# Kernel optimization log

Measured on AMD Instinct MI355X. Metric: run time of the kernel, lower is better.

The kernel has to match this reference:

```python
import jax, jax.numpy as jnp
import numpy as np
from jax import lax

B, D, K = 256, 128, 8192


def _conv_same(x, w, b):
    # x: [B,C,H,W], w: [O,I,3,3] (torch Conv2d layout), stride 1, padding 1 == SAME
    y = lax.conv_general_dilated(x, w, (1, 1), 'SAME',
                                 dimension_numbers=('NCHW', 'OIHW', 'NCHW'))
    return y + b[None, :, None, None]


def _convT_same(x, w, b):
    # torch ConvTranspose2d(k=3, stride=1, padding=1) with weight [I,O,3,3]
    # == SAME conv with spatially flipped kernel and swapped in/out channels
    wt = jnp.flip(w, axis=(2, 3)).transpose(1, 0, 2, 3)  # -> [O,I,3,3]
    return _conv_same(x, wt, b)


def setup_inputs() -> dict:
    key = jax.random.key(0)
    ks = jax.random.split(key, 12)
    s = 0.05
    return {
        'patch':  jax.random.normal(ks[0], (B, 3, 64, 64), jnp.float32),
        'enc_w1': jax.random.normal(ks[1], (64, 3, 3, 3), jnp.float32) * s,
        'enc_b1': jnp.zeros((64,), jnp.float32),
        'enc_w2': jax.random.normal(ks[2], (D, 64, 3, 3), jnp.float32) * s,
        'enc_b2': jnp.zeros((D,), jnp.float32),
        'emb':    jax.random.normal(ks[3], (K, D), jnp.float32),
        'dec_w1': jax.random.normal(ks[4], (D, 64, 3, 3), jnp.float32) * s,  # ConvT [in,out,k,k]
        'dec_b1': jnp.zeros((64,), jnp.float32),
        'dec_w2': jax.random.normal(ks[5], (64, 64, 3, 3), jnp.float32) * s,
        'dec_b2': jnp.zeros((64,), jnp.float32),
        'dec_w3': jax.random.normal(ks[6], (64, 3, 3, 3), jnp.float32) * s,
        'dec_b3': jnp.zeros((3,), jnp.float32),
    }


def reference(patch, enc_w1, enc_b1, enc_w2, enc_b2, emb,
              dec_w1, dec_b1, dec_w2, dec_b2, dec_w3, dec_b3):
    # ---- encode_patch ----
    h = jax.nn.relu(_conv_same(patch, enc_w1, enc_b1))
    h = _conv_same(h, enc_w2, enc_b2)
    z = jnp.mean(h, axis=(2, 3))  # AdaptiveAvgPool2d((1,1)) + flatten -> [B,D]

    # ---- VQ: cdist + argmin + gather ----
    # argmin over squared L2 == argmin over cdist(p=2); avoid sqrt.
    d2 = (jnp.sum(z * z, axis=1, keepdims=True)
          + jnp.sum(emb * emb, axis=1)[None, :]
          - 2.0 * z @ emb.T)  # [B,K]
    encoding_indices = jnp.argmin(d2, axis=1)  # [B]
    z_q = emb[encoding_indices]  # [B,D]

    commitment_loss = jnp.mean((lax.stop_gradient(z_q) - z) ** 2)
    codebook_loss = jnp.mean((z_q - lax.stop_gradient(z)) ** 2)

    # ---- decode_vector ----
    # bilinear interpolate of a 1x1 map to 64x64 is a pure broadcast
    v = jnp.broadcast_to(z_q[:, :, None, None], (z_q.shape[0], z_q.shape[1], 64, 64))
    d = jax.nn.relu(_convT_same(v, dec_w1, dec_b1))
    d = jax.nn.relu(_convT_same(d, dec_w2, dec_b2))
    recon = jnp.tanh(_convT_same(d, dec_w3, dec_b3))  # [B,3,64,64]

    return recon, codebook_loss, commitment_loss, encoding_indices[:, None]
```

## Files before the change

### kernel.cpp

```cpp
#include <hip/hip_runtime.h>
#include <math.h>

typedef float float4u __attribute__((ext_vector_type(4), aligned(4)));


__global__ __launch_bounds__(512) void k_conv_z(
    const float* __restrict__ patch, const float* __restrict__ w1,
    const float* __restrict__ b1, const float* __restrict__ w2,
    const float* __restrict__ b2, const float* __restrict__ dw1,
    const float* __restrict__ emb,
    float* __restrict__ z, float* __restrict__ zn2,
    float* __restrict__ Wcfg, float* __restrict__ en2)
{
    __shared__ __align__(16) float lds[14256];
    const int blk = blockIdx.x, tid = threadIdx.x;

    if (blk >= 256) {
        const int gid = (blk - 256) * 512 + tid;
        if (gid < 73728) {
            const int cfg = gid >> 13;
            const int o = (gid >> 7) & 63;
            const int i = gid & 127;
            const int cy = cfg / 3, cx = cfg % 3;
            const int ylo = (cy == 2) ? 1 : 0, yhi = (cy == 0) ? 1 : 2;
            const int xlo = (cx == 2) ? 1 : 0, xhi = (cx == 0) ? 1 : 2;
            const float* wp = dw1 + ((size_t)i * 64 + o) * 9;
            float s = 0.f;
            for (int ky = ylo; ky <= yhi; ++ky)
                for (int kx = xlo; kx <= xhi; ++kx)
                    s += wp[ky * 3 + kx];
            Wcfg[gid] = s;
        } else {
            const int k = gid - 73728;
            const float4* e = (const float4*)(emb + (size_t)k * 128);
            float s = 0.f;
            for (int t = 0; t < 32; ++t) {
                const float4 v = e[t];
                s = fmaf(v.x, v.x, fmaf(v.y, v.y, fmaf(v.z, v.z, fmaf(v.w, v.w, s))));
            }
            en2[k] = s;
        }
        return;
    }

    const float* pb = patch + (size_t)blk * 12288;
    for (int i = tid; i < 14256; i += 512) {
        const int c = i / 4752, rem = i - c * 4752;
        const int r = rem / 72, p = rem - r * 72;
        const int y = r - 1, x = p - 3;
        float v = 0.f;
        if (y >= 0 && y < 64 && x >= 0 && x < 64)
            v = pb[(c << 12) + (y << 6) + x];
        lds[i] = v;
    }
    __syncthreads();

    const int ch = tid & 63, q = tid >> 6;
    float w[3][3][3];
#pragma unroll
    for (int ic = 0; ic < 3; ++ic)
#pragma unroll
        for (int ky = 0; ky < 3; ++ky)
#pragma unroll
            for (int kx = 0; kx < 3; ++kx)
                w[ic][ky][kx] = w1[((ch * 3 + ic) * 3 + ky) * 3 + kx];
    const float bias = b1[ch];

    float T = 0, r0s = 0, r63s = 0, c0s = 0, c63s = 0;
    float h00 = 0, h063 = 0, h630 = 0, h6363 = 0;

#pragma unroll 1
    for (int r8 = 0; r8 < 8; ++r8) {
        const int y = q * 8 + r8;
#pragma unroll 1
        for (int m = 0; m < 8; ++m) {
            float a[8];
#pragma unroll
            for (int j = 0; j < 8; ++j) a[j] = bias;
#pragma unroll
            for (int ic = 0; ic < 3; ++ic)
#pragma unroll
                for (int ky = 0; ky < 3; ++ky) {
                    const float* rowp = &lds[(ic * 66 + y + ky) * 72 + m * 8 + 2];
                    const float2 f01 = *(const float2*)rowp;
                    const float4 f25 = *(const float4*)(rowp + 2);
                    const float4 f69 = *(const float4*)(rowp + 6);
                    const float f[10] = {f01.x, f01.y, f25.x, f25.y, f25.z, f25.w,
                                         f69.x, f69.y, f69.z, f69.w};
                    const float w0 = w[ic][ky][0], w1v = w[ic][ky][1], w2v = w[ic][ky][2];
#pragma unroll
                    for (int j = 0; j < 8; ++j)
                        a[j] = fmaf(w0, f[j], fmaf(w1v, f[j + 1], fmaf(w2v, f[j + 2], a[j])));
                }
#pragma unroll
            for (int j = 0; j < 8; ++j) a[j] = fmaxf(a[j], 0.f);
            const float rs = ((a[0] + a[1]) + (a[2] + a[3])) + ((a[4] + a[5]) + (a[6] + a[7]));
            T += rs;
            if (y == 0)  { r0s += rs;  if (m == 0) h00 = a[0];  if (m == 7) h063 = a[7]; }
            if (y == 63) { r63s += rs; if (m == 0) h630 = a[0]; if (m == 7) h6363 = a[7]; }
            if (m == 0) c0s += a[0];
            if (m == 7) c63s += a[7];
        }
    }
    __syncthreads();

    {
        const float st[9] = {T, r0s, r63s, c0s, c63s, h00, h063, h630, h6363};
#pragma unroll
        for (int s = 0; s < 9; ++s) lds[(s * 8 + q) * 64 + ch] = st[s];
    }
    __syncthreads();

    float* Ssh = lds + 4608;
    if (tid < 64) {
        float f[9];
#pragma unroll
        for (int s = 0; s < 9; ++s) {
            float v = 0.f;
#pragma unroll
            for (int g = 0; g < 8; ++g) v += lds[(s * 8 + g) * 64 + tid];
            f[s] = v;
        }
        const float Tt = f[0], R0 = f[1], R63 = f[2], C0 = f[3], C63 = f[4];
        const float H00 = f[5], H063 = f[6], H630 = f[7], H6363 = f[8];
#pragma unroll
        for (int ky = 0; ky < 3; ++ky) {
            const float rex = (ky == 0) ? R63 : (ky == 2 ? R0 : 0.f);
#pragma unroll
            for (int kx = 0; kx < 3; ++kx) {
                const float cex = (kx == 0) ? C63 : (kx == 2 ? C0 : 0.f);
                float corner = 0.f;
                if (ky == 0 && kx == 0) corner = H6363;
                if (ky == 0 && kx == 2) corner = H630;
                if (ky == 2 && kx == 0) corner = H063;
                if (ky == 2 && kx == 2) corner = H00;
                Ssh[tid * 9 + ky * 3 + kx] = (Tt - rex - cex + corner) * (1.f / 4096.f);
            }
        }
    }
    __syncthreads();

    float* zp = lds + 5184;
    {
        const int oc = tid & 127, h = tid >> 7;
        const float4* Wv = (const float4*)(w2 + (size_t)oc * 576 + h * 144);
        const float4* Sv = (const float4*)(Ssh + h * 144);
        float acc = 0.f;
        for (int t = 0; t < 36; ++t) {
            const float4 w4 = Wv[t], s4 = Sv[t];
            acc = fmaf(w4.x, s4.x, acc);
            acc = fmaf(w4.y, s4.y, acc);
            acc = fmaf(w4.z, s4.z, acc);
            acc = fmaf(w4.w, s4.w, acc);
        }
        zp[tid] = acc;
    }
    __syncthreads();
    float* red2 = lds + 5696;
    if (tid < 128) {
        const float zv = b2[tid] + ((zp[tid] + zp[tid + 128]) + (zp[tid + 256] + zp[tid + 384]));
        z[(size_t)blk * 128 + tid] = zv;
        red2[tid] = zv * zv;
    }
    __syncthreads();
    if (tid < 64) {
        float v = red2[tid] + red2[tid + 64];
        v += __shfl_xor(v, 32); v += __shfl_xor(v, 16); v += __shfl_xor(v, 8);
        v += __shfl_xor(v, 4);  v += __shfl_xor(v, 2);  v += __shfl_xor(v, 1);
        if (tid == 0) zn2[blk] = v;
    }
}

__global__ __launch_bounds__(256) void k_vq(
    const float* __restrict__ z, const float* __restrict__ emb,
    const float* __restrict__ en2, float* __restrict__ pd2, int* __restrict__ pidx)
{
    __shared__ __align__(16) float zsh[1024];
    __shared__ float wd[8][4];
    __shared__ int   wi[8][4];
    const int tid = threadIdx.x;
    const int bg = blockIdx.x >> 4, kc = blockIdx.x & 15;
    const int b0 = bg * 8;
    for (int i = tid; i < 1024; i += 256) zsh[i] = z[(size_t)b0 * 128 + i];
    __syncthreads();

    const int k0 = kc * 512 + tid, k1 = k0 + 256;
    const float4* e0 = (const float4*)(emb + (size_t)k0 * 128);
    const float4* e1 = (const float4*)(emb + (size_t)k1 * 128);
    const float4* zv = (const float4*)zsh;

    float acc0[8], acc1[8];
#pragma unroll
    for (int bb = 0; bb < 8; ++bb) { acc0[bb] = 0.f; acc1[bb] = 0.f; }

    for (int t = 0; t < 32; ++t) {
        const float4 ea = e0[t], eb = e1[t];
#pragma unroll
        for (int bb = 0; bb < 8; ++bb) {
            const float4 zz = zv[bb * 32 + t];
            acc0[bb] = fmaf(zz.x, ea.x, fmaf(zz.y, ea.y, fmaf(zz.z, ea.z, fmaf(zz.w, ea.w, acc0[bb]))));
            acc1[bb] = fmaf(zz.x, eb.x, fmaf(zz.y, eb.y, fmaf(zz.z, eb.z, fmaf(zz.w, eb.w, acc1[bb]))));
        }
    }
    const float E0 = en2[k0], E1 = en2[k1];
    const int wv_ = tid >> 6, ln = tid & 63;
#pragma unroll
    for (int bb = 0; bb < 8; ++bb) {
        const float da = fmaf(-2.f, acc0[bb], E0);
        const float db = fmaf(-2.f, acc1[bb], E1);
        float d; int ix;
        if (da <= db) { d = da; ix = k0; } else { d = db; ix = k1; }
#pragma unroll
        for (int off = 32; off > 0; off >>= 1) {
            const float od = __shfl_xor(d, off);
            const int   oi = __shfl_xor(ix, off);
            if (od < d || (od == d && oi < ix)) { d = od; ix = oi; }
        }
        if (ln == 0) { wd[bb][wv_] = d; wi[bb][wv_] = ix; }
    }
    __syncthreads();
    if (tid < 8) {
        float d = wd[tid][0]; int ix = wi[tid][0];
#pragma unroll
        for (int wv2 = 1; wv2 < 4; ++wv2) {
            const float od = wd[tid][wv2]; const int oi = wi[tid][wv2];
            if (od < d || (od == d && oi < ix)) { d = od; ix = oi; }
        }
        pd2[(b0 + tid) * 16 + kc] = d;
        pidx[(b0 + tid) * 16 + kc] = ix;
    }
}

__global__ __launch_bounds__(256) void k_stage1(
    const float* __restrict__ emb, const float* __restrict__ zn2,
    const float* __restrict__ pd2, const int* __restrict__ pidx,
    const float* __restrict__ Wcfg, const float* __restrict__ db1,
    float* __restrict__ d1all, float* __restrict__ out)
{
    __shared__ float wsl[64 * 132];
    __shared__ float zql[8 * 132];
    __shared__ int   bish[8];
    __shared__ float redl[256];
    const int tid = threadIdx.x;
    const int g = blockIdx.x / 9, c = blockIdx.x - g * 9;
    const int b0 = g * 8;

    float dmin = pd2[tid * 16]; int bi = pidx[tid * 16];
    for (int j = 1; j < 16; ++j) {
        const float d = pd2[tid * 16 + j]; const int ix = pidx[tid * 16 + j];
        if (d < dmin || (d == dmin && ix < bi)) { dmin = d; bi = ix; }
    }
    if (tid >= b0 && tid < b0 + 8) bish[tid - b0] = bi;
    redl[tid] = dmin + zn2[tid];
    __syncthreads();
    if (blockIdx.x == 0) out[3145730 + tid] = (float)bi;
    if (tid < 128) redl[tid] += redl[tid + 128];
    __syncthreads();
    if (tid < 64) {
        float v = redl[tid] + redl[tid + 64];
        v += __shfl_xor(v, 32); v += __shfl_xor(v, 16); v += __shfl_xor(v, 8);
        v += __shfl_xor(v, 4);  v += __shfl_xor(v, 2);  v += __shfl_xor(v, 1);
        if (tid == 0 && blockIdx.x == 0) {
            const float L = v * (1.f / 32768.f);
            out[3145728] = L;
            out[3145729] = L;
        }
    }

    for (int idx = tid; idx < 2048; idx += 256) {
        const int o = idx >> 5, k4 = idx & 31;
        *(float4*)&wsl[o * 132 + k4 * 4] =
            *(const float4*)&Wcfg[((size_t)c * 64 + o) * 128 + k4 * 4];
    }
    {
        const int b = tid >> 5, k4 = tid & 31;
        *(float4*)&zql[b * 132 + k4 * 4] =
            *(const float4*)&emb[(size_t)bish[b] * 128 + k4 * 4];
    }
    __syncthreads();

#pragma unroll
    for (int pp = 0; pp < 2; ++pp) {
        const int pair = tid + pp * 256;
        const int o = pair >> 3, bb = pair & 7;
        const float4* wv = (const float4*)&wsl[o * 132];
        const float4* zv = (const float4*)&zql[bb * 132];
        float acc = db1[o];
        for (int t = 0; t < 32; ++t) {
            const float4 w4 = wv[t], z4 = zv[t];
            acc = fmaf(w4.x, z4.x, acc);
            acc = fmaf(w4.y, z4.y, acc);
            acc = fmaf(w4.z, z4.z, acc);
            acc = fmaf(w4.w, z4.w, acc);
        }
        d1all[((size_t)(b0 + bb)) * 576 + o * 9 + c] = fmaxf(acc, 0.f);
    }
}

__global__ __launch_bounds__(256) void k_decode(
    const float* __restrict__ d1all, const float* __restrict__ dw2,
    const float* __restrict__ db2, const float* __restrict__ dw3,
    const float* __restrict__ db3, float* __restrict__ out)
{
    __shared__ float d1e[64][10];
    __shared__ float d2e[64][26];
    __shared__ float o3[3 * 49];
    __shared__ float dw3sh[1728];

    const int b = blockIdx.x, tid = threadIdx.x;
    for (int id = tid; id < 576; id += 256) d1e[id / 9][id % 9] = d1all[(size_t)b * 576 + id];
    for (int id = tid; id < 1728; id += 256) dw3sh[id] = dw3[id];
    if (tid < 64) { d1e[tid][9] = 0.f; d2e[tid][25] = 0.f; }
    __syncthreads();

    {
        const int TY5[5][3] = {{-1,0,1},{0,1,1},{1,1,1},{1,1,2},{1,2,-1}};
        const int o = tid >> 2, isub = tid & 3;
        float acc[25];
#pragma unroll
        for (int cc = 0; cc < 25; ++cc) acc[cc] = 0.f;
        for (int ii = 0; ii < 16; ++ii) {
            const int i = isub + ii * 4;
            float d1v[10];
#pragma unroll
            for (int t = 0; t < 9; ++t) d1v[t] = d1e[i][t];
            d1v[9] = 0.f;
            const float* wp = dw2 + ((size_t)i * 64 + o) * 9;
            const float4u w03 = *(const float4u*)wp;
            const float4u w47 = *(const float4u*)(wp + 4);
            const float w8v = wp[8];
            const float w9[9] = {w03.x, w03.y, w03.z, w03.w, w47.x, w47.y, w47.z, w47.w, w8v};
#pragma unroll
            for (int cy = 0; cy < 5; ++cy) {
#pragma unroll
                for (int ky = 0; ky < 3; ++ky) {
                    const int ty = TY5[cy][ky];
                    if (ty < 0) continue;
#pragma unroll
                    for (int cx = 0; cx < 5; ++cx) {
#pragma unroll
                        for (int kx = 0; kx < 3; ++kx) {
                            const int tx = TY5[cx][kx];
                            if (tx < 0) continue;
                            acc[cy * 5 + cx] = fmaf(w9[(2 - ky) * 3 + (2 - kx)],
                                                    d1v[ty * 3 + tx], acc[cy * 5 + cx]);
                        }
                    }
                }
            }
        }
#pragma unroll
        for (int cc = 0; cc < 25; ++cc) {
            float v = acc[cc];
            v += __shfl_xor(v, 1);
            v += __shfl_xor(v, 2);
            if (isub == 0) d2e[o][cc] = fmaxf(v + db2[o], 0.f);
        }
    }
    __syncthreads();

    if (tid < 147) {
        const int TY7[7][3] = {{-1,0,1},{0,1,2},{1,2,2},{2,2,2},{2,2,3},{2,3,4},{3,4,-1}};
        const int c3 = tid / 49, cc = tid % 49, cy = cc / 7, cx = cc % 7;
        float acc = db3[c3];
        for (int i = 0; i < 64; ++i) {
            const float* wp = &dw3sh[(i * 3 + c3) * 9];
#pragma unroll
            for (int ky = 0; ky < 3; ++ky) {
                const int ty = TY7[cy][ky];
#pragma unroll
                for (int kx = 0; kx < 3; ++kx) {
                    const int tx = TY7[cx][kx];
                    const int t = (ty < 0 || tx < 0) ? 25 : ty * 5 + tx;
                    acc = fmaf(wp[(2 - ky) * 3 + (2 - kx)], d2e[i][t], acc);
                }
            }
        }
        o3[c3 * 49 + cc] = tanhf(acc);
    }
    __syncthreads();

    float4* ob = (float4*)(out + (size_t)b * 12288);
    for (int id = tid; id < 3072; id += 256) {
        const int base = id * 4;
        const int c = base >> 12, rem = base & 4095, y = rem >> 6, x0 = rem & 63;
        const int ry = (y <= 3) ? y : (y >= 60 ? y - 57 : 3);
        const float* row = &o3[c * 49 + ry * 7];
        float4 v;
        int x;
        x = x0 + 0; v.x = row[(x <= 3) ? x : (x >= 60 ? x - 57 : 3)];
        x = x0 + 1; v.y = row[(x <= 3) ? x : (x >= 60 ? x - 57 : 3)];
        x = x0 + 2; v.z = row[(x <= 3) ? x : (x >= 60 ? x - 57 : 3)];
        x = x0 + 3; v.w = row[(x <= 3) ? x : (x >= 60 ? x - 57 : 3)];
        ob[id] = v;
    }
}

extern "C" void kernel_launch(void* const* d_in, const int* in_sizes, int n_in,
                              void* d_out, int out_size, void* d_ws, size_t ws_size,
                              hipStream_t stream)
{
    const float* patch  = (const float*)d_in[0];
    const float* enc_w1 = (const float*)d_in[1];
    const float* enc_b1 = (const float*)d_in[2];
    const float* enc_w2 = (const float*)d_in[3];
    const float* enc_b2 = (const float*)d_in[4];
    const float* emb    = (const float*)d_in[5];
    const float* dec_w1 = (const float*)d_in[6];
    const float* dec_b1 = (const float*)d_in[7];
    const float* dec_w2 = (const float*)d_in[8];
    const float* dec_b2 = (const float*)d_in[9];
    const float* dec_w3 = (const float*)d_in[10];
    const float* dec_b3 = (const float*)d_in[11];

    float* out = (float*)d_out;
    float* ws  = (float*)d_ws;

    float* z     = ws;
    float* zn2   = ws + 32768;
    float* pd2   = ws + 33024;
    int*   pidx  = (int*)(ws + 37120);
    float* Wcfg  = ws + 41216;
    float* en2   = ws + 114944;
    float* d1all = ws + 123136;

    k_conv_z<<<dim3(416), dim3(512), 0, stream>>>(patch, enc_w1, enc_b1, enc_w2, enc_b2,
                                                  dec_w1, emb, z, zn2, Wcfg, en2);
    k_vq<<<dim3(512), dim3(256), 0, stream>>>(z, emb, en2, pd2, pidx);
    k_stage1<<<dim3(288), dim3(256), 0, stream>>>(emb, zn2, pd2, pidx, Wcfg, dec_b1,
                                                  d1all, out);
    k_decode<<<dim3(256), dim3(256), 0, stream>>>(d1all, dec_w2, dec_b2, dec_w3,
                                                  dec_b3, out);
}
```

Measured before the change: 146.8 us.

## Split encoder conv across four row-group blocks and fuse stage1 into decode

The first encoder conv is now split so each image is handled by four 256-thread blocks, one per 16-row group. Each block writes partial statistics to a workspace buffer, and the last block to finish (found via an atomic counter) reduces them and computes z. The conv inner loop is re-tiled to compute 4x4 output register tiles with row reuse. The separate stage1 kernel is merged into the decode kernel, which drops one launch and the d1all round trip, at the cost of per-sample redundant argmin reduction and a matvec that reads Wcfg straight from global memory. A memset is added to reset the counters.

```diff
diff --git a/kernel.cpp b/kernel.cpp
--- a/kernel.cpp
+++ b/kernel.cpp
@@ -4,19 +4,21 @@
 typedef float float4u __attribute__((ext_vector_type(4), aligned(4)));
 
 
-__global__ __launch_bounds__(512) void k_conv_z(
+__global__ __launch_bounds__(256, 3) void k_conv_z(
     const float* __restrict__ patch, const float* __restrict__ w1,
     const float* __restrict__ b1, const float* __restrict__ w2,
     const float* __restrict__ b2, const float* __restrict__ dw1,
     const float* __restrict__ emb,
+    float* __restrict__ pstat, int* __restrict__ cnt,
     float* __restrict__ z, float* __restrict__ zn2,
     float* __restrict__ Wcfg, float* __restrict__ en2)
 {
-    __shared__ __align__(16) float lds[14256];
+    __shared__ __align__(16) float lds[3888];
+    __shared__ int winflag;
     const int blk = blockIdx.x, tid = threadIdx.x;
 
-    if (blk >= 256) {
-        const int gid = (blk - 256) * 512 + tid;
+    if (blk >= 1024) {
+        const int gid = (blk - 1024) * 256 + tid;
         if (gid < 73728) {
             const int cfg = gid >> 13;
             const int o = (gid >> 7) & 63;
@@ -30,7 +32,7 @@
                 for (int kx = xlo; kx <= xhi; ++kx)
                     s += wp[ky * 3 + kx];
             Wcfg[gid] = s;
-        } else {
+        } else if (gid < 81920) {
             const int k = gid - 73728;
             const float4* e = (const float4*)(emb + (size_t)k * 128);
             float s = 0.f;
@@ -43,11 +45,13 @@
         return;
     }
 
-    const float* pb = patch + (size_t)blk * 12288;
-    for (int i = tid; i < 14256; i += 512) {
-        const int c = i / 4752, rem = i - c * 4752;
+    const int b = blk >> 2, rg = blk & 3;
+    const int y0 = rg * 16;
+    const float* pb = patch + (size_t)b * 12288;
+    for (int i = tid; i < 3888; i += 256) {
+        const int c = i / 1296, rem = i - c * 1296;
         const int r = rem / 72, p = rem - r * 72;
-        const int y = r - 1, x = p - 3;
+        const int y = y0 + r - 1, x = p - 3;
         float v = 0.f;
         if (y >= 0 && y < 64 && x >= 0 && x < 64)
             v = pb[(c << 12) + (y << 6) + x];
@@ -56,73 +60,99 @@
     __syncthreads();
 
     const int ch = tid & 63, q = tid >> 6;
-    float w[3][3][3];
+    float wgt[3][3][3];
 #pragma unroll
     for (int ic = 0; ic < 3; ++ic)
 #pragma unroll
         for (int ky = 0; ky < 3; ++ky)
 #pragma unroll
             for (int kx = 0; kx < 3; ++kx)
-                w[ic][ky][kx] = w1[((ch * 3 + ic) * 3 + ky) * 3 + kx];
+                wgt[ic][ky][kx] = w1[((ch * 3 + ic) * 3 + ky) * 3 + kx];
     const float bias = b1[ch];
+    const bool top = (rg == 0) && (q == 0);
+    const bool bot = (rg == 3) && (q == 3);
 
     float T = 0, r0s = 0, r63s = 0, c0s = 0, c63s = 0;
     float h00 = 0, h063 = 0, h630 = 0, h6363 = 0;
+    const float* tb = lds + q * 288;
 
 #pragma unroll 1
-    for (int r8 = 0; r8 < 8; ++r8) {
-        const int y = q * 8 + r8;
-#pragma unroll 1
-        for (int m = 0; m < 8; ++m) {
-            float a[8];
-#pragma unroll
-            for (int j = 0; j < 8; ++j) a[j] = bias;
-#pragma unroll
-            for (int ic = 0; ic < 3; ++ic)
-#pragma unroll
-                for (int ky = 0; ky < 3; ++ky) {
-                    const float* rowp = &lds[(ic * 66 + y + ky) * 72 + m * 8 + 2];
-                    const float2 f01 = *(const float2*)rowp;
-                    const float4 f25 = *(const float4*)(rowp + 2);
-                    const float4 f69 = *(const float4*)(rowp + 6);
-                    const float f[10] = {f01.x, f01.y, f25.x, f25.y, f25.z, f25.w,
-                                         f69.x, f69.y, f69.z, f69.w};
-                    const float w0 = w[ic][ky][0], w1v = w[ic][ky][1], w2v = w[ic][ky][2];
-#pragma unroll
-                    for (int j = 0; j < 8; ++j)
-                        a[j] = fmaf(w0, f[j], fmaf(w1v, f[j + 1], fmaf(w2v, f[j + 2], a[j])));
+    for (int xc = 0; xc < 16; ++xc) {
+        const float* bp = tb + xc * 4;
+        float acc[4][4];
+#pragma unroll
+        for (int dr = 0; dr < 4; ++dr)
+#pragma unroll
+            for (int j = 0; j < 4; ++j) acc[dr][j] = bias;
+
+#pragma unroll
+        for (int ic = 0; ic < 3; ++ic) {
+#pragma unroll
+            for (int rr = 0; rr < 6; ++rr) {
+                const float2 f01 = *(const float2*)(bp + (ic * 18 + rr) * 72 + 2);
+                const float4 f25 = *(const float4*)(bp + (ic * 18 + rr) * 72 + 4);
+                const float w6[6] = {f01.x, f01.y, f25.x, f25.y, f25.z, f25.w};
+#pragma unroll
+                for (int dr = 0; dr < 4; ++dr) {
+                    const int ky = rr - dr;
+                    if (ky >= 0 && ky < 3) {
+                        const float wa = wgt[ic][ky][0], wb = wgt[ic][ky][1], wc = wgt[ic][ky][2];
+#pragma unroll
+                        for (int j = 0; j < 4; ++j)
+                            acc[dr][j] = fmaf(wa, w6[j], fmaf(wb, w6[j + 1],
+                                          fmaf(wc, w6[j + 2], acc[dr][j])));
+                    }
                 }
-#pragma unroll
-            for (int j = 0; j < 8; ++j) a[j] = fmaxf(a[j], 0.f);
-            const float rs = ((a[0] + a[1]) + (a[2] + a[3])) + ((a[4] + a[5]) + (a[6] + a[7]));
-            T += rs;
-            if (y == 0)  { r0s += rs;  if (m == 0) h00 = a[0];  if (m == 7) h063 = a[7]; }
-            if (y == 63) { r63s += rs; if (m == 0) h630 = a[0]; if (m == 7) h6363 = a[7]; }
-            if (m == 0) c0s += a[0];
-            if (m == 7) c63s += a[7];
-        }
+            }
+        }
+        float rs[4];
+#pragma unroll
+        for (int dr = 0; dr < 4; ++dr) {
+#pragma unroll
+            for (int j = 0; j < 4; ++j) acc[dr][j] = fmaxf(acc[dr][j], 0.f);
+            rs[dr] = (acc[dr][0] + acc[dr][1]) + (acc[dr][2] + acc[dr][3]);
+            T += rs[dr];
+        }
+        if (xc == 0)  c0s  += (acc[0][0] + acc[1][0]) + (acc[2][0] + acc[3][0]);
+        if (xc == 15) c63s += (acc[0][3] + acc[1][3]) + (acc[2][3] + acc[3][3]);
+        if (top) { r0s += rs[0];  if (xc == 0) h00 = acc[0][0];  if (xc == 15) h063 = acc[0][3]; }
+        if (bot) { r63s += rs[3]; if (xc == 0) h630 = acc[3][0]; if (xc == 15) h6363 = acc[3][3]; }
     }
     __syncthreads();
 
     {
         const float st[9] = {T, r0s, r63s, c0s, c63s, h00, h063, h630, h6363};
 #pragma unroll
-        for (int s = 0; s < 9; ++s) lds[(s * 8 + q) * 64 + ch] = st[s];
-    }
-    __syncthreads();
-
-    float* Ssh = lds + 4608;
+        for (int s = 0; s < 9; ++s) lds[(s * 4 + q) * 64 + ch] = st[s];
+    }
+    __syncthreads();
     if (tid < 64) {
-        float f[9];
-#pragma unroll
-        for (int s = 0; s < 9; ++s) {
-            float v = 0.f;
-#pragma unroll
-            for (int g = 0; g < 8; ++g) v += lds[(s * 8 + g) * 64 + tid];
-            f[s] = v;
-        }
-        const float Tt = f[0], R0 = f[1], R63 = f[2], C0 = f[3], C63 = f[4];
-        const float H00 = f[5], H063 = f[6], H630 = f[7], H6363 = f[8];
+        float* pp = pstat + (size_t)blk * 576;
+#pragma unroll
+        for (int s = 0; s < 9; ++s)
+            pp[s * 64 + tid] = (lds[(s * 4 + 0) * 64 + tid] + lds[(s * 4 + 1) * 64 + tid])
+                             + (lds[(s * 4 + 2) * 64 + tid] + lds[(s * 4 + 3) * 64 + tid]);
+    }
+    __threadfence();
+    __syncthreads();
+    if (tid == 0) winflag = (atomicAdd(&cnt[b], 1) == 3) ? 1 : 0;
+    __syncthreads();
+    if (!winflag) return;
+    __threadfence();
+
+    const volatile float* vp = pstat + (size_t)b * 2304;
+    for (int i = tid; i < 576; i += 256) {
+        float s = (vp[i] + vp[576 + i]) + (vp[1152 + i] + vp[1728 + i]);
+        lds[i] = s;
+    }
+    __syncthreads();
+
+    float* Ssh = lds + 576;
+    if (tid < 64) {
+        const float Tt   = lds[0 * 64 + tid], R0  = lds[1 * 64 + tid], R63 = lds[2 * 64 + tid];
+        const float C0   = lds[3 * 64 + tid], C63 = lds[4 * 64 + tid];
+        const float H00  = lds[5 * 64 + tid], H063 = lds[6 * 64 + tid];
+        const float H630 = lds[7 * 64 + tid], H6363 = lds[8 * 64 + tid];
 #pragma unroll
         for (int ky = 0; ky < 3; ++ky) {
             const float rex = (ky == 0) ? R63 : (ky == 2 ? R0 : 0.f);
@@ -140,13 +170,13 @@
     }
     __syncthreads();
 
-    float* zp = lds + 5184;
+    float* zp = lds + 1152;
     {
         const int oc = tid & 127, h = tid >> 7;
-        const float4* Wv = (const float4*)(w2 + (size_t)oc * 576 + h * 144);
-        const float4* Sv = (const float4*)(Ssh + h * 144);
+        const float4* Wv = (const float4*)(w2 + (size_t)oc * 576 + h * 288);
+        const float4* Sv = (const float4*)(Ssh + h * 288);
         float acc = 0.f;
-        for (int t = 0; t < 36; ++t) {
+        for (int t = 0; t < 72; ++t) {
             const float4 w4 = Wv[t], s4 = Sv[t];
             acc = fmaf(w4.x, s4.x, acc);
             acc = fmaf(w4.y, s4.y, acc);
@@ -156,10 +186,10 @@
         zp[tid] = acc;
     }
     __syncthreads();
-    float* red2 = lds + 5696;
+    float* red2 = lds + 1408;
     if (tid < 128) {
-        const float zv = b2[tid] + ((zp[tid] + zp[tid + 128]) + (zp[tid + 256] + zp[tid + 384]));
-        z[(size_t)blk * 128 + tid] = zv;
+        const float zv = b2[tid] + zp[tid] + zp[tid + 128];
+        z[(size_t)b * 128 + tid] = zv;
         red2[tid] = zv * zv;
     }
     __syncthreads();
@@ -167,7 +197,7 @@
         float v = red2[tid] + red2[tid + 64];
         v += __shfl_xor(v, 32); v += __shfl_xor(v, 16); v += __shfl_xor(v, 8);
         v += __shfl_xor(v, 4);  v += __shfl_xor(v, 2);  v += __shfl_xor(v, 1);
-        if (tid == 0) zn2[blk] = v;
+        if (tid == 0) zn2[b] = v;
     }
 }
 
@@ -231,60 +261,57 @@
     }
 }
 
-__global__ __launch_bounds__(256) void k_stage1(
+__global__ __launch_bounds__(256) void k_decode(
     const float* __restrict__ emb, const float* __restrict__ zn2,
     const float* __restrict__ pd2, const int* __restrict__ pidx,
     const float* __restrict__ Wcfg, const float* __restrict__ db1,
-    float* __restrict__ d1all, float* __restrict__ out)
+    const float* __restrict__ dw2, const float* __restrict__ db2,
+    const float* __restrict__ dw3, const float* __restrict__ db3,
+    float* __restrict__ out)
 {
-    __shared__ float wsl[64 * 132];
-    __shared__ float zql[8 * 132];
-    __shared__ int   bish[8];
+    __shared__ __align__(16) float zsh[128];
+    __shared__ float d1e[64][10];
+    __shared__ float d2e[64][26];
+    __shared__ float o3[3 * 49];
+    __shared__ float dw3sh[1728];
     __shared__ float redl[256];
-    const int tid = threadIdx.x;
-    const int g = blockIdx.x / 9, c = blockIdx.x - g * 9;
-    const int b0 = g * 8;
+    __shared__ int bsel;
+
+    const int b = blockIdx.x, tid = threadIdx.x;
 
     float dmin = pd2[tid * 16]; int bi = pidx[tid * 16];
     for (int j = 1; j < 16; ++j) {
         const float d = pd2[tid * 16 + j]; const int ix = pidx[tid * 16 + j];
         if (d < dmin || (d == dmin && ix < bi)) { dmin = d; bi = ix; }
     }
-    if (tid >= b0 && tid < b0 + 8) bish[tid - b0] = bi;
+    if (tid == b) bsel = bi;
     redl[tid] = dmin + zn2[tid];
     __syncthreads();
-    if (blockIdx.x == 0) out[3145730 + tid] = (float)bi;
-    if (tid < 128) redl[tid] += redl[tid + 128];
-    __syncthreads();
+
+    if (b == 0) out[3145730 + tid] = (float)bi;
+    if (tid < 128) {
+        redl[tid] += redl[tid + 128];
+        zsh[tid] = emb[(size_t)bsel * 128 + tid];
+    }
+    for (int id = tid; id < 1728; id += 256) dw3sh[id] = dw3[id];
+    if (tid < 64) { d1e[tid][9] = 0.f; d2e[tid][25] = 0.f; }
+    __syncthreads();
+
     if (tid < 64) {
         float v = redl[tid] + redl[tid + 64];
         v += __shfl_xor(v, 32); v += __shfl_xor(v, 16); v += __shfl_xor(v, 8);
         v += __shfl_xor(v, 4);  v += __shfl_xor(v, 2);  v += __shfl_xor(v, 1);
-        if (tid == 0 && blockIdx.x == 0) {
+        if (tid == 0 && b == 0) {
             const float L = v * (1.f / 32768.f);
             out[3145728] = L;
             out[3145729] = L;
         }
     }
 
-    for (int idx = tid; idx < 2048; idx += 256) {
-        const int o = idx >> 5, k4 = idx & 31;
-        *(float4*)&wsl[o * 132 + k4 * 4] =
-            *(const float4*)&Wcfg[((size_t)c * 64 + o) * 128 + k4 * 4];
-    }
-    {
-        const int b = tid >> 5, k4 = tid & 31;
-        *(float4*)&zql[b * 132 + k4 * 4] =
-            *(const float4*)&emb[(size_t)bish[b] * 128 + k4 * 4];
-    }
-    __syncthreads();
-
-#pragma unroll
-    for (int pp = 0; pp < 2; ++pp) {
-        const int pair = tid + pp * 256;
-        const int o = pair >> 3, bb = pair & 7;
-        const float4* wv = (const float4*)&wsl[o * 132];
-        const float4* zv = (const float4*)&zql[bb * 132];
+    for (int id = tid; id < 576; id += 256) {
+        const int o = id / 9, cfg = id - o * 9;
+        const float4* wv = (const float4*)(Wcfg + ((size_t)cfg * 64 + o) * 128);
+        const float4* zv = (const float4*)zsh;
         float acc = db1[o];
         for (int t = 0; t < 32; ++t) {
             const float4 w4 = wv[t], z4 = zv[t];
@@ -293,24 +320,8 @@
             acc = fmaf(w4.z, z4.z, acc);
             acc = fmaf(w4.w, z4.w, acc);
         }
-        d1all[((size_t)(b0 + bb)) * 576 + o * 9 + c] = fmaxf(acc, 0.f);
-    }
-}
-
-__global__ __launch_bounds__(256) void k_decode(
-    const float* __restrict__ d1all, const float* __restrict__ dw2,
-    const float* __restrict__ db2, const float* __restrict__ dw3,
-    const float* __restrict__ db3, float* __restrict__ out)
-{
-    __shared__ float d1e[64][10];
-    __shared__ float d2e[64][26];
-    __shared__ float o3[3 * 49];
-    __shared__ float dw3sh[1728];
-
-    const int b = blockIdx.x, tid = threadIdx.x;
-    for (int id = tid; id < 576; id += 256) d1e[id / 9][id % 9] = d1all[(size_t)b * 576 + id];
-    for (int id = tid; id < 1728; id += 256) dw3sh[id] = dw3[id];
-    if (tid < 64) { d1e[tid][9] = 0.f; d2e[tid][25] = 0.f; }
+        d1e[o][cfg] = fmaxf(acc, 0.f);
+    }
     __syncthreads();
 
     {
@@ -416,19 +427,20 @@
     float* out = (float*)d_out;
     float* ws  = (float*)d_ws;
 
-    float* z     = ws;
-    float* zn2   = ws + 32768;
-    float* pd2   = ws + 33024;
-    int*   pidx  = (int*)(ws + 37120);
-    float* Wcfg  = ws + 41216;
-    float* en2   = ws + 114944;
-    float* d1all = ws + 123136;
-
-    k_conv_z<<<dim3(416), dim3(512), 0, stream>>>(patch, enc_w1, enc_b1, enc_w2, enc_b2,
-                                                  dec_w1, emb, z, zn2, Wcfg, en2);
+    float* pstat = ws;
+    float* z     = ws + 589824;
+    float* zn2   = ws + 622592;
+    float* pd2   = ws + 622848;
+    int*   pidx  = (int*)(ws + 626944);
+    float* Wcfg  = ws + 631040;
+    float* en2   = ws + 704768;
+    int*   cnt   = (int*)(ws + 712960);
+
+    hipMemsetAsync(cnt, 0, 256 * sizeof(int), stream);
+
+    k_conv_z<<<dim3(1344), dim3(256), 0, stream>>>(patch, enc_w1, enc_b1, enc_w2, enc_b2,
+                                                   dec_w1, emb, pstat, cnt, z, zn2, Wcfg, en2);
     k_vq<<<dim3(512), dim3(256), 0, stream>>>(z, emb, en2, pd2, pidx);
-    k_stage1<<<dim3(288), dim3(256), 0, stream>>>(emb, zn2, pd2, pidx, Wcfg, dec_b1,
-                                                  d1all, out);
-    k_decode<<<dim3(256), dim3(256), 0, stream>>>(d1all, dec_w2, dec_b2, dec_w3,
-                                                  dec_b3, out);
+    k_decode<<<dim3(256), dim3(256), 0, stream>>>(emb, zn2, pd2, pidx, Wcfg, dec_b1,
+                                                  dec_w2, dec_b2, dec_w3, dec_b3, out);
 }
```

Measured after the change: 244.9 us. +66.8%, slower.
